# Optimization experiments

Hardware: AMD Instinct MI355X
Metric: run time of the kernel (lower is better)

Reference implementation:

```python
import jax, jax.numpy as jnp
import numpy as np

N, G, NPG = 8192, 128, 64        # total nodes, graphs, nodes per graph
D_IN, H, D_OUT = 128, 128, 10
DEG = 16                          # avg degree -> E = N*DEG
K = int(NPG * 0.5)                # keep_ratio = 0.5 -> topk per graph


def setup_inputs() -> dict:
    key = jax.random.key(0)
    ks = jax.random.split(key, 20)
    E = N * DEG
    # within-graph random edges (graphs are contiguous blocks of NPG nodes)
    src = jax.random.randint(ks[0], (E,), 0, NPG)
    dst = jax.random.randint(ks[1], (E,), 0, NPG)
    offs = jnp.repeat(jnp.arange(G, dtype=jnp.int32) * NPG, NPG * DEG)
    edge_index = jnp.stack([src.astype(jnp.int32) + offs, dst.astype(jnp.int32) + offs])
    batch = jnp.repeat(jnp.arange(G, dtype=jnp.int32), NPG)
    x = jax.random.normal(ks[2], (N, D_IN), jnp.float32)

    def lin(k, i, o):
        return jax.random.normal(k, (i, o), jnp.float32) * (1.0 / np.sqrt(i))

    return {
        "x": x, "edge_index": edge_index, "batch": batch,
        "W1": lin(ks[3], D_IN, H), "b1": jnp.zeros((H,), jnp.float32),
        "W2": lin(ks[4], H, H),    "b2": jnp.zeros((H,), jnp.float32),
        "W3": lin(ks[5], H, H),    "b3": jnp.zeros((H,), jnp.float32),
        "Wa": lin(ks[6], 3 * H, 1), "ba": jnp.zeros((1,), jnp.float32),
        "M1": lin(ks[7], 6 * H, H),      "c1": jnp.zeros((H,), jnp.float32),
        "M2": lin(ks[8], H, H // 2),     "c2": jnp.zeros((H // 2,), jnp.float32),
        "M3": lin(ks[9], H // 2, D_OUT), "c3": jnp.zeros((D_OUT,), jnp.float32),
    }


def reference(x, edge_index, batch, W1, b1, W2, b2, W3, b3, Wa, ba,
              M1, c1, M2, c2, M3, c3):
    n = x.shape[0]
    # generate_adjacency: dense [N,N] from edge list (symmetrized)
    A = jnp.zeros((n, n), x.dtype).at[edge_index[0], edge_index[1]].set(1.0)
    A = jnp.maximum(A, A.T)
    # normalize_adjacency: D^{-1/2} (A + I) D^{-1/2}
    A = A + jnp.eye(n, dtype=x.dtype)
    dinv = jax.lax.rsqrt(A.sum(axis=1))
    A = A * dinv[:, None] * dinv[None, :]

    gcn = lambda X, W, b: A @ (X @ W) + b
    h1 = jax.nn.relu(gcn(x, W1, b1))
    h2 = jax.nn.relu(gcn(h1, W2, b2))
    h3 = jax.nn.relu(gcn(h2, W3, b3))
    feats = jnp.concatenate([h1, h2, h3], axis=1)          # [N, 3H]

    # SelfAttentionPooling: GCN attention score + tanh + per-graph topk
    score = jnp.tanh((A @ (feats @ Wa) + ba)[:, 0])        # [N]
    s = score.reshape(G, NPG)                              # [G, NPG]
    _, idx = jax.lax.top_k(s, K)                           # [G, K]
    fg = feats.reshape(G, NPG, 3 * H)
    sel = jnp.take_along_axis(fg, idx[..., None], axis=1)  # [G, K, 3H]
    ssel = jnp.take_along_axis(s, idx, axis=1)             # [G, K]
    masked = sel * ssel[..., None]

    # Readout: mean || max per graph -> [G, 6H]
    readout = jnp.concatenate([masked.mean(axis=1), masked.max(axis=1)], axis=1)

    # MLP (dropout inactive at inference)
    h = jax.nn.relu(readout @ M1 + c1)
    h = jax.nn.relu(h @ M2 + c2)
    return h @ M3 + c3                                     # [G, D_OUT]
```

## Files before the change

kernel.cpp:

```cpp
#include <hip/hip_runtime.h>


#define NGRAPH 128
#define EPG    1024
#define ETOT   131072
#define DIM    128
#define KSEL   32
#define SA     68
#define SF     132

#define O_A    0
#define O_B0   4352
#define O_B1   12800
#define O_PPAR 21248
#define O_PRE  22272
#define O_SC   22336
#define O_SEL  22400
#define LDS_FLOATS 22464
#define LDS_BYTES  (LDS_FLOATS * 4)
#define O_RO   O_B0
#define O_MH   (O_B0 + 768)
#define O_HM   (O_B0 + 1792)
#define O_H2M  (O_B0 + 1920)

#define FMA8(A, xs, w0, w1) do { \
  A[0] += (xs)*(w0).x; A[1] += (xs)*(w0).y; A[2] += (xs)*(w0).z; A[3] += (xs)*(w0).w; \
  A[4] += (xs)*(w1).x; A[5] += (xs)*(w1).y; A[6] += (xs)*(w1).z; A[7] += (xs)*(w1).w; } while(0)

__device__ __forceinline__ float rdlane(float v, int lane) {
  return __int_as_float(__builtin_amdgcn_readlane(__float_as_int(v), lane));
}

__device__ void gcn_layer(float* lds, const float* Bin, float* Bout,
                          const float* __restrict__ Wg,
                          const float* __restrict__ bg,
                          const float* __restrict__ waCol,
                          float* __restrict__ Hg, int tid)
{
  float* sA   = lds + O_A;
  float* ppar = lds + O_PPAR;
  float* pre  = lds + O_PRE;
  const int r  = tid & 63;
  const int w  = tid >> 6;
  const int c0 = __builtin_amdgcn_readfirstlane(w * 8);

  float acc[8] = {0.f,0.f,0.f,0.f,0.f,0.f,0.f,0.f};
  const float* wp = Wg + c0;
  #pragma unroll 2
  for (int kq = 0; kq < 32; ++kq) {
    float4 xv = *(const float4*)&Bin[r * SF + kq * 4];
    const float* wr = wp + (kq * 4) * DIM;
    float4 w00 = *(const float4*)&wr[0];
    float4 w01 = *(const float4*)&wr[4];
    float4 w10 = *(const float4*)&wr[DIM];
    float4 w11 = *(const float4*)&wr[DIM + 4];
    float4 w20 = *(const float4*)&wr[2 * DIM];
    float4 w21 = *(const float4*)&wr[2 * DIM + 4];
    float4 w30 = *(const float4*)&wr[3 * DIM];
    float4 w31 = *(const float4*)&wr[3 * DIM + 4];
    FMA8(acc, xv.x, w00, w01);
    FMA8(acc, xv.y, w10, w11);
    FMA8(acc, xv.z, w20, w21);
    FMA8(acc, xv.w, w30, w31);
  }

  float4 bv0 = *(const float4*)&bg[c0];
  float4 bv1 = *(const float4*)&bg[c0 + 4];
  float h[8];
  h[0] = bv0.x; h[1] = bv0.y; h[2] = bv0.z; h[3] = bv0.w;
  h[4] = bv1.x; h[5] = bv1.y; h[6] = bv1.z; h[7] = bv1.w;
  for (int jq = 0; jq < 16; ++jq) {
    float4 a4 = *(const float4*)&sA[r * SA + jq * 4];
    #pragma unroll
    for (int jj = 0; jj < 4; ++jj) {
      const int lane = jq * 4 + jj;
      const float aj = (jj == 0) ? a4.x : (jj == 1) ? a4.y
                     : (jj == 2) ? a4.z : a4.w;
      #pragma unroll
      for (int c = 0; c < 8; ++c)
        h[c] += aj * rdlane(acc[c], lane);
    }
  }
  float4 o0, o1;
  o0.x = fmaxf(h[0], 0.f); o0.y = fmaxf(h[1], 0.f);
  o0.z = fmaxf(h[2], 0.f); o0.w = fmaxf(h[3], 0.f);
  o1.x = fmaxf(h[4], 0.f); o1.y = fmaxf(h[5], 0.f);
  o1.z = fmaxf(h[6], 0.f); o1.w = fmaxf(h[7], 0.f);
  *(float4*)&Bout[r * SF + c0]     = o0;
  *(float4*)&Bout[r * SF + c0 + 4] = o1;
  *(float4*)&Hg[r * DIM + c0]      = o0;
  *(float4*)&Hg[r * DIM + c0 + 4]  = o1;
  float4 wa0 = *(const float4*)&waCol[c0];
  float4 wa1 = *(const float4*)&waCol[c0 + 4];
  ppar[w * 64 + r] = o0.x*wa0.x + o0.y*wa0.y + o0.z*wa0.z + o0.w*wa0.w
                   + o1.x*wa1.x + o1.y*wa1.y + o1.z*wa1.z + o1.w*wa1.w;
  __syncthreads();
  if (tid < 64) {
    float s = 0.f;
    #pragma unroll
    for (int q = 0; q < 16; ++q) s += ppar[q * 64 + tid];
    pre[tid] += s;
  }
  __syncthreads();
}

extern "C" __global__ void __launch_bounds__(1024)
sagpool(const float* __restrict__ x,  const int* __restrict__ ei,
        const float* __restrict__ W1, const float* __restrict__ b1,
        const float* __restrict__ W2, const float* __restrict__ b2,
        const float* __restrict__ W3, const float* __restrict__ b3,
        const float* __restrict__ Wa, const float* __restrict__ ba,
        const float* __restrict__ M1, const float* __restrict__ c1,
        const float* __restrict__ M2, const float* __restrict__ c2,
        const float* __restrict__ M3, const float* __restrict__ c3,
        float* __restrict__ h1w, float* __restrict__ h2w,
        float* __restrict__ h3w, float* __restrict__ out)
{
  extern __shared__ float lds[];
  const int g = blockIdx.x, tid = threadIdx.x;
  float* sA  = lds + O_A;
  float* B0  = lds + O_B0;
  float* B1  = lds + O_B1;
  float* pre = lds + O_PRE;
  float* sc  = lds + O_SC;
  float* sel = lds + O_SEL;
  float* ro  = lds + O_RO;
  float* mh  = lds + O_MH;
  float* hm  = lds + O_HM;
  float* h2m = lds + O_H2M;

  for (int i = tid; i < 64 * SA; i += 1024) sA[i] = 0.f;
  if (tid < 64) pre[tid] = 0.f;
  __syncthreads();
  {
    int s = ei[g * EPG + tid] & 63;
    int d = ei[ETOT + g * EPG + tid] & 63;
    sA[s * SA + d] = 1.0f;
    sA[d * SA + s] = 1.0f;
  }
  __syncthreads();
  if (tid < 64) sA[tid * SA + tid] += 1.0f;
  __syncthreads();
  {
    int r = tid >> 4, q = tid & 15;
    float sum = sA[r * SA + q * 4]     + sA[r * SA + q * 4 + 1]
              + sA[r * SA + q * 4 + 2] + sA[r * SA + q * 4 + 3];
    sum += __shfl_xor(sum, 1);
    sum += __shfl_xor(sum, 2);
    sum += __shfl_xor(sum, 4);
    sum += __shfl_xor(sum, 8);
    if (q == 0) sc[r] = 1.0f / sqrtf(sum);
  }
  __syncthreads();
  for (int i = tid; i < 4096; i += 1024) {
    int r = i >> 6, c = i & 63;
    sA[r * SA + c] *= sc[r] * sc[c];
  }
  {
    const float4* xg = (const float4*)(x + g * 64 * DIM);
    for (int i = tid; i < 2048; i += 1024) {
      int r = i >> 5, q = i & 31;
      *(float4*)&B0[r * SF + q * 4] = xg[i];
    }
  }
  __syncthreads();

  gcn_layer(lds, B0, B1, W1, b1, Wa,           h1w + g * 8192, tid);
  gcn_layer(lds, B1, B0, W2, b2, Wa + DIM,     h2w + g * 8192, tid);
  gcn_layer(lds, B0, B1, W3, b3, Wa + 2 * DIM, h3w + g * 8192, tid);

  {
    int r = tid >> 4, q = tid & 15;
    float p = sA[r * SA + q * 4]     * pre[q * 4]
            + sA[r * SA + q * 4 + 1] * pre[q * 4 + 1]
            + sA[r * SA + q * 4 + 2] * pre[q * 4 + 2]
            + sA[r * SA + q * 4 + 3] * pre[q * 4 + 3];
    p += __shfl_xor(p, 1);
    p += __shfl_xor(p, 2);
    p += __shfl_xor(p, 4);
    p += __shfl_xor(p, 8);
    if (q == 0) sc[r] = tanhf(p + ba[0]);
  }
  __syncthreads();

  if (tid < 64) {
    float mys = sc[tid];
    int cnt = 0;
    for (int j = 0; j < 64; ++j) {
      float sj = sc[j];
      cnt += (sj > mys || (sj == mys && j < tid)) ? 1 : 0;
    }
    sel[tid] = (cnt < KSEL) ? 1.0f : 0.0f;
  }
  __syncthreads();

  if (tid < 768) {
    int c = tid >> 1, half = tid & 1;
    int which = c >> 7, cc = c & 127;
    const float* hb = ((which == 0) ? h1w : (which == 1) ? h2w : h3w) + g * 8192;
    float sum = 0.f, mx = -1e30f;
    for (int i = half * 32; i < half * 32 + 32; ++i) {
      if (sel[i] > 0.5f) {
        float v = sc[i] * hb[i * DIM + cc];
        sum += v;
        mx = fmaxf(mx, v);
      }
    }
    sum += __shfl_xor(sum, 1);
    mx = fmaxf(mx, __shfl_xor(mx, 1));
    if (half == 0) {
      ro[c]       = sum * (1.0f / KSEL);
      ro[384 + c] = mx;
    }
  }
  __syncthreads();

  {
    int j = tid & 127, oc = tid >> 7;
    float a = 0.f;
    int k0 = oc * 96;
    for (int k = k0; k < k0 + 96; k += 4) {
      float4 r4 = *(const float4*)&ro[k];
      a += r4.x * M1[(k + 0) * DIM + j];
      a += r4.y * M1[(k + 1) * DIM + j];
      a += r4.z * M1[(k + 2) * DIM + j];
      a += r4.w * M1[(k + 3) * DIM + j];
    }
    mh[oc * 128 + j] = a;
  }
  __syncthreads();
  if (tid < 128) {
    float v = c1[tid];
    #pragma unroll
    for (int q = 0; q < 8; ++q) v += mh[q * 128 + tid];
    hm[tid] = fmaxf(v, 0.f);
  }
  __syncthreads();
  if (tid < 64) {
    float a = c2[tid];
    for (int k = 0; k < 128; ++k) a += hm[k] * M2[k * 64 + tid];
    h2m[tid] = fmaxf(a, 0.f);
  }
  __syncthreads();
  if (tid < 10) {
    float a = c3[tid];
    for (int k = 0; k < 64; ++k) a += h2m[k] * M3[k * 10 + tid];
    out[g * 10 + tid] = a;
  }
}

extern "C" void kernel_launch(void* const* d_in, const int* in_sizes, int n_in,
                              void* d_out, int out_size, void* d_ws, size_t ws_size,
                              hipStream_t stream) {
  const float* x  = (const float*)d_in[0];
  const int*   ei = (const int*)d_in[1];
  const float* W1 = (const float*)d_in[3];
  const float* b1 = (const float*)d_in[4];
  const float* W2 = (const float*)d_in[5];
  const float* b2 = (const float*)d_in[6];
  const float* W3 = (const float*)d_in[7];
  const float* b3 = (const float*)d_in[8];
  const float* Wa = (const float*)d_in[9];
  const float* ba = (const float*)d_in[10];
  const float* M1 = (const float*)d_in[11];
  const float* c1 = (const float*)d_in[12];
  const float* M2 = (const float*)d_in[13];
  const float* c2 = (const float*)d_in[14];
  const float* M3 = (const float*)d_in[15];
  const float* c3 = (const float*)d_in[16];
  float* out = (float*)d_out;

  float* ws  = (float*)d_ws;
  float* h1w = ws;
  float* h2w = ws + 1048576;
  float* h3w = ws + 2097152;

  (void)hipFuncSetAttribute(reinterpret_cast<const void*>(sagpool),
                            hipFuncAttributeMaxDynamicSharedMemorySize, LDS_BYTES);
  sagpool<<<NGRAPH, 1024, LDS_BYTES, stream>>>(x, ei, W1, b1, W2, b2, W3, b3,
                                               Wa, ba, M1, c1, M2, c2, M3, c3,
                                               h1w, h2w, h3w, out);
}
```

Before: 154.6 us.

## Split fused per-graph kernel into per-layer launches with two column-half blocks

Replaces the single 128-block, 1024-thread kernel with three per-layer launches of 256 blocks (two per graph, each computing 64 output columns), plus a final pooling/MLP kernel. The normalized adjacency is built once in layer 1 and stored to workspace for reuse, and activations round-trip through global memory between layers. This doubles block count to fill more CUs on the device, at the cost of extra launches, global traffic for activations and adjacency, and duplicated adjacency/X loads per half.

```diff
diff --git a/kernel.cpp b/kernel.cpp
--- a/kernel.cpp
+++ b/kernel.cpp
@@ -9,19 +9,11 @@
 #define SA     68
 #define SF     132
 
-#define O_A    0
-#define O_B0   4352
-#define O_B1   12800
-#define O_PPAR 21248
-#define O_PRE  22272
-#define O_SC   22336
-#define O_SEL  22400
-#define LDS_FLOATS 22464
-#define LDS_BYTES  (LDS_FLOATS * 4)
-#define O_RO   O_B0
-#define O_MH   (O_B0 + 768)
-#define O_HM   (O_B0 + 1792)
-#define O_H2M  (O_B0 + 1920)
+#define WS_A    0
+#define WS_H1   524288
+#define WS_H2   1572864
+#define WS_H3   2621440
+#define WS_PREP 3670016
 
 #define FMA8(A, xs, w0, w1) do { \
   A[0] += (xs)*(w0).x; A[1] += (xs)*(w0).y; A[2] += (xs)*(w0).z; A[3] += (xs)*(w0).w; \
@@ -31,24 +23,85 @@
   return __int_as_float(__builtin_amdgcn_readlane(__float_as_int(v), lane));
 }
 
-__device__ void gcn_layer(float* lds, const float* Bin, float* Bout,
-                          const float* __restrict__ Wg,
-                          const float* __restrict__ bg,
-                          const float* __restrict__ waCol,
-                          float* __restrict__ Hg, int tid)
+__global__ void __launch_bounds__(512)
+k_layer(const float* __restrict__ Xsrc, const int* __restrict__ ei,
+        float* __restrict__ wsA, const float* __restrict__ Wg,
+        const float* __restrict__ bg, const float* __restrict__ waCol,
+        float* __restrict__ Hg, float* __restrict__ preP,
+        const int build_adj, const int first)
 {
-  float* sA   = lds + O_A;
-  float* ppar = lds + O_PPAR;
-  float* pre  = lds + O_PRE;
+  __shared__ float sA[64 * SA];
+  __shared__ float sX[64 * SF];
+  __shared__ float ppar[512];
+  __shared__ float dv[64];
+  const int g   = blockIdx.x >> 1;
+  const int ch  = blockIdx.x & 1;
+  const int tid = threadIdx.x;
+
+  if (build_adj) {
+    for (int i = tid; i < 64 * SA; i += 512) sA[i] = 0.f;
+    __syncthreads();
+    {
+      const int* srcp = ei + g * EPG;
+      const int* dstp = ei + ETOT + g * EPG;
+      #pragma unroll
+      for (int t = 0; t < 2; ++t) {
+        int e = tid + t * 512;
+        int s = srcp[e] & 63;
+        int d = dstp[e] & 63;
+        sA[s * SA + d] = 1.0f;
+        sA[d * SA + s] = 1.0f;
+      }
+    }
+    __syncthreads();
+    if (tid < 64) sA[tid * SA + tid] += 1.0f;
+    __syncthreads();
+    if (tid < 256) {
+      int r = tid >> 2, q = tid & 3;
+      float sum = 0.f;
+      int jb = q * 16;
+      #pragma unroll
+      for (int j = 0; j < 16; ++j) sum += sA[r * SA + jb + j];
+      sum += __shfl_xor(sum, 1);
+      sum += __shfl_xor(sum, 2);
+      if (q == 0) dv[r] = 1.0f / sqrtf(sum);
+    }
+    __syncthreads();
+    for (int i = tid; i < 4096; i += 512) {
+      int r = i >> 6, c = i & 63;
+      sA[r * SA + c] *= dv[r] * dv[c];
+    }
+    __syncthreads();
+    if (ch == 0) {
+      float* outA = wsA + g * 4096;
+      for (int i = tid; i < 4096; i += 512)
+        outA[i] = sA[(i >> 6) * SA + (i & 63)];
+    }
+  } else {
+    const float4* asrc = (const float4*)(wsA + g * 4096);
+    for (int i = tid; i < 1024; i += 512) {
+      int r = i >> 4, c4 = i & 15;
+      *(float4*)&sA[r * SA + c4 * 4] = asrc[i];
+    }
+  }
+  {
+    const float4* s = (const float4*)(Xsrc + g * 8192);
+    for (int i = tid; i < 2048; i += 512) {
+      int r = i >> 5, q = i & 31;
+      *(float4*)&sX[r * SF + q * 4] = s[i];
+    }
+  }
+  __syncthreads();
+
   const int r  = tid & 63;
   const int w  = tid >> 6;
-  const int c0 = __builtin_amdgcn_readfirstlane(w * 8);
+  const int c0 = __builtin_amdgcn_readfirstlane(ch * 64 + w * 8);
 
   float acc[8] = {0.f,0.f,0.f,0.f,0.f,0.f,0.f,0.f};
   const float* wp = Wg + c0;
-  #pragma unroll 2
+  #pragma unroll 4
   for (int kq = 0; kq < 32; ++kq) {
-    float4 xv = *(const float4*)&Bin[r * SF + kq * 4];
+    float4 xv = *(const float4*)&sX[r * SF + kq * 4];
     const float* wr = wp + (kq * 4) * DIM;
     float4 w00 = *(const float4*)&wr[0];
     float4 w01 = *(const float4*)&wr[4];
@@ -86,10 +139,8 @@
   o0.z = fmaxf(h[2], 0.f); o0.w = fmaxf(h[3], 0.f);
   o1.x = fmaxf(h[4], 0.f); o1.y = fmaxf(h[5], 0.f);
   o1.z = fmaxf(h[6], 0.f); o1.w = fmaxf(h[7], 0.f);
-  *(float4*)&Bout[r * SF + c0]     = o0;
-  *(float4*)&Bout[r * SF + c0 + 4] = o1;
-  *(float4*)&Hg[r * DIM + c0]      = o0;
-  *(float4*)&Hg[r * DIM + c0 + 4]  = o1;
+  *(float4*)&Hg[(g * 64 + r) * DIM + c0]     = o0;
+  *(float4*)&Hg[(g * 64 + r) * DIM + c0 + 4] = o1;
   float4 wa0 = *(const float4*)&waCol[c0];
   float4 wa1 = *(const float4*)&waCol[c0 + 4];
   ppar[w * 64 + r] = o0.x*wa0.x + o0.y*wa0.y + o0.z*wa0.z + o0.w*wa0.w
@@ -98,143 +149,80 @@
   if (tid < 64) {
     float s = 0.f;
     #pragma unroll
-    for (int q = 0; q < 16; ++q) s += ppar[q * 64 + tid];
-    pre[tid] += s;
-  }
-  __syncthreads();
-}
-
-extern "C" __global__ void __launch_bounds__(1024)
-sagpool(const float* __restrict__ x,  const int* __restrict__ ei,
-        const float* __restrict__ W1, const float* __restrict__ b1,
-        const float* __restrict__ W2, const float* __restrict__ b2,
-        const float* __restrict__ W3, const float* __restrict__ b3,
-        const float* __restrict__ Wa, const float* __restrict__ ba,
+    for (int q = 0; q < 8; ++q) s += ppar[q * 64 + tid];
+    float* pp = preP + (ch * NGRAPH + g) * 64 + tid;
+    if (first) *pp = s; else *pp += s;
+  }
+}
+
+__global__ void __launch_bounds__(256)
+k_final(const float* __restrict__ wsA, const float* __restrict__ preP,
+        const float* __restrict__ h1g, const float* __restrict__ h2g,
+        const float* __restrict__ h3g, const float* __restrict__ ba,
         const float* __restrict__ M1, const float* __restrict__ c1,
         const float* __restrict__ M2, const float* __restrict__ c2,
         const float* __restrict__ M3, const float* __restrict__ c3,
-        float* __restrict__ h1w, float* __restrict__ h2w,
-        float* __restrict__ h3w, float* __restrict__ out)
+        float* __restrict__ out)
 {
-  extern __shared__ float lds[];
+  __shared__ float spre[64], ssc[64], ssel[64];
+  __shared__ float ro[768], mh[256], hm[128], h2m[64];
   const int g = blockIdx.x, tid = threadIdx.x;
-  float* sA  = lds + O_A;
-  float* B0  = lds + O_B0;
-  float* B1  = lds + O_B1;
-  float* pre = lds + O_PRE;
-  float* sc  = lds + O_SC;
-  float* sel = lds + O_SEL;
-  float* ro  = lds + O_RO;
-  float* mh  = lds + O_MH;
-  float* hm  = lds + O_HM;
-  float* h2m = lds + O_H2M;
-
-  for (int i = tid; i < 64 * SA; i += 1024) sA[i] = 0.f;
-  if (tid < 64) pre[tid] = 0.f;
+
+  if (tid < 64)
+    spre[tid] = preP[g * 64 + tid] + preP[(NGRAPH + g) * 64 + tid];
   __syncthreads();
   {
-    int s = ei[g * EPG + tid] & 63;
-    int d = ei[ETOT + g * EPG + tid] & 63;
-    sA[s * SA + d] = 1.0f;
-    sA[d * SA + s] = 1.0f;
-  }
-  __syncthreads();
-  if (tid < 64) sA[tid * SA + tid] += 1.0f;
-  __syncthreads();
-  {
-    int r = tid >> 4, q = tid & 15;
-    float sum = sA[r * SA + q * 4]     + sA[r * SA + q * 4 + 1]
-              + sA[r * SA + q * 4 + 2] + sA[r * SA + q * 4 + 3];
-    sum += __shfl_xor(sum, 1);
-    sum += __shfl_xor(sum, 2);
-    sum += __shfl_xor(sum, 4);
-    sum += __shfl_xor(sum, 8);
-    if (q == 0) sc[r] = 1.0f / sqrtf(sum);
-  }
-  __syncthreads();
-  for (int i = tid; i < 4096; i += 1024) {
-    int r = i >> 6, c = i & 63;
-    sA[r * SA + c] *= sc[r] * sc[c];
-  }
-  {
-    const float4* xg = (const float4*)(x + g * 64 * DIM);
-    for (int i = tid; i < 2048; i += 1024) {
-      int r = i >> 5, q = i & 31;
-      *(float4*)&B0[r * SF + q * 4] = xg[i];
-    }
-  }
-  __syncthreads();
-
-  gcn_layer(lds, B0, B1, W1, b1, Wa,           h1w + g * 8192, tid);
-  gcn_layer(lds, B1, B0, W2, b2, Wa + DIM,     h2w + g * 8192, tid);
-  gcn_layer(lds, B0, B1, W3, b3, Wa + 2 * DIM, h3w + g * 8192, tid);
-
-  {
-    int r = tid >> 4, q = tid & 15;
-    float p = sA[r * SA + q * 4]     * pre[q * 4]
-            + sA[r * SA + q * 4 + 1] * pre[q * 4 + 1]
-            + sA[r * SA + q * 4 + 2] * pre[q * 4 + 2]
-            + sA[r * SA + q * 4 + 3] * pre[q * 4 + 3];
+    int r = tid >> 2, q = tid & 3;
+    const float* Ar = wsA + g * 4096 + r * 64;
+    float p = 0.f;
+    int jb = q * 16;
+    #pragma unroll
+    for (int j = 0; j < 16; ++j) p += Ar[jb + j] * spre[jb + j];
     p += __shfl_xor(p, 1);
     p += __shfl_xor(p, 2);
-    p += __shfl_xor(p, 4);
-    p += __shfl_xor(p, 8);
-    if (q == 0) sc[r] = tanhf(p + ba[0]);
-  }
-  __syncthreads();
-
+    if (q == 0) ssc[r] = tanhf(p + ba[0]);
+  }
+  __syncthreads();
   if (tid < 64) {
-    float mys = sc[tid];
+    float mys = ssc[tid];
     int cnt = 0;
     for (int j = 0; j < 64; ++j) {
-      float sj = sc[j];
+      float sj = ssc[j];
       cnt += (sj > mys || (sj == mys && j < tid)) ? 1 : 0;
     }
-    sel[tid] = (cnt < KSEL) ? 1.0f : 0.0f;
-  }
-  __syncthreads();
-
-  if (tid < 768) {
-    int c = tid >> 1, half = tid & 1;
+    ssel[tid] = (cnt < KSEL) ? 1.0f : 0.0f;
+  }
+  __syncthreads();
+  for (int c = tid; c < 384; c += 256) {
     int which = c >> 7, cc = c & 127;
-    const float* hb = ((which == 0) ? h1w : (which == 1) ? h2w : h3w) + g * 8192;
+    const float* hb = ((which == 0) ? h1g : (which == 1) ? h2g : h3g) + g * 8192;
     float sum = 0.f, mx = -1e30f;
-    for (int i = half * 32; i < half * 32 + 32; ++i) {
-      if (sel[i] > 0.5f) {
-        float v = sc[i] * hb[i * DIM + cc];
+    for (int i = 0; i < 64; ++i) {
+      if (ssel[i] > 0.5f) {
+        float v = ssc[i] * hb[i * DIM + cc];
         sum += v;
         mx = fmaxf(mx, v);
       }
     }
-    sum += __shfl_xor(sum, 1);
-    mx = fmaxf(mx, __shfl_xor(mx, 1));
-    if (half == 0) {
-      ro[c]       = sum * (1.0f / KSEL);
-      ro[384 + c] = mx;
-    }
-  }
-  __syncthreads();
-
+    ro[c]       = sum * (1.0f / KSEL);
+    ro[384 + c] = mx;
+  }
+  __syncthreads();
   {
-    int j = tid & 127, oc = tid >> 7;
+    int j = tid & 127, half = tid >> 7;
     float a = 0.f;
-    int k0 = oc * 96;
-    for (int k = k0; k < k0 + 96; k += 4) {
+    int k0 = half * 384;
+    for (int k = k0; k < k0 + 384; k += 4) {
       float4 r4 = *(const float4*)&ro[k];
       a += r4.x * M1[(k + 0) * DIM + j];
       a += r4.y * M1[(k + 1) * DIM + j];
       a += r4.z * M1[(k + 2) * DIM + j];
       a += r4.w * M1[(k + 3) * DIM + j];
     }
-    mh[oc * 128 + j] = a;
-  }
-  __syncthreads();
-  if (tid < 128) {
-    float v = c1[tid];
-    #pragma unroll
-    for (int q = 0; q < 8; ++q) v += mh[q * 128 + tid];
-    hm[tid] = fmaxf(v, 0.f);
-  }
+    mh[half * 128 + j] = a;
+  }
+  __syncthreads();
+  if (tid < 128) hm[tid] = fmaxf(mh[tid] + mh[128 + tid] + c1[tid], 0.f);
   __syncthreads();
   if (tid < 64) {
     float a = c2[tid];
@@ -270,14 +258,19 @@
   const float* c3 = (const float*)d_in[16];
   float* out = (float*)d_out;
 
-  float* ws  = (float*)d_ws;
-  float* h1w = ws;
-  float* h2w = ws + 1048576;
-  float* h3w = ws + 2097152;
-
-  (void)hipFuncSetAttribute(reinterpret_cast<const void*>(sagpool),
-                            hipFuncAttributeMaxDynamicSharedMemorySize, LDS_BYTES);
-  sagpool<<<NGRAPH, 1024, LDS_BYTES, stream>>>(x, ei, W1, b1, W2, b2, W3, b3,
-                                               Wa, ba, M1, c1, M2, c2, M3, c3,
-                                               h1w, h2w, h3w, out);
-}
+  float* ws   = (float*)d_ws;
+  float* wsA  = ws + WS_A;
+  float* h1w  = ws + WS_H1;
+  float* h2w  = ws + WS_H2;
+  float* h3w  = ws + WS_H3;
+  float* preP = ws + WS_PREP;
+
+  k_layer<<<2 * NGRAPH, 512, 0, stream>>>(x,   ei, wsA, W1, b1, Wa,
+                                          h1w, preP, 1, 1);
+  k_layer<<<2 * NGRAPH, 512, 0, stream>>>(h1w, ei, wsA, W2, b2, Wa + DIM,
+                                          h2w, preP, 0, 0);
+  k_layer<<<2 * NGRAPH, 512, 0, stream>>>(h2w, ei, wsA, W3, b3, Wa + 2 * DIM,
+                                          h3w, preP, 0, 0);
+  k_final<<<NGRAPH, 256, 0, stream>>>(wsA, preP, h1w, h2w, h3w, ba,
+                                      M1, c1, M2, c2, M3, c3, out);
+}
```

New measurement: 171.0 us. 10.6% more time.
